# Kernel tuning notes

Hardware: AMD Instinct MI355X
Metric: run time of the kernel (lower is better)

Reference implementation:

```python
import jax, jax.numpy as jnp
import numpy as np

DIM = 2048
N_HEADS = 16
HEAD_DIM = DIM // N_HEADS  # 128
MAX_LEN = 2048
B, T = 2, 2048
RESTORE_SCALE = DIM ** 0.5  # sqkinit / sqkscale = 1 / (1/sqrt(dim))
SQK_SCALE = 1.0 / DIM ** 0.5


def _rope_tables(seq_len, head_dim, dtype=jnp.float32):
    d2 = head_dim // 2
    pos = jnp.arange(seq_len, dtype=dtype)                     # [T]
    theta = 1.0 / (10000.0 ** (jnp.arange(0, head_dim, 2, dtype=dtype) / head_dim))  # [d2]
    ang = pos[:, None] * theta[None, :]                        # [T, d2]
    return jnp.cos(ang), jnp.sin(ang)


def _apply_rope(x, cos, sin):
    # x: [B, H, T, D]; cos/sin: [T, D/2] broadcast over B,H
    d2 = x.shape[-1] // 2
    xr, xi = x[..., :d2], x[..., d2:]
    return jnp.concatenate([xr * cos - xi * sin, xr * sin + xi * cos], axis=-1)


def setup_inputs() -> dict:
    key = jax.random.key(0)
    ks = jax.random.split(key, 5)
    s = 0.02
    return {
        "x":  jax.random.normal(ks[0], (B, T, DIM), jnp.float32),
        "Wq": jax.random.normal(ks[1], (DIM, DIM), jnp.float32) * s,
        "Wk": jax.random.normal(ks[2], (DIM, DIM), jnp.float32) * s,
        "Wv": jax.random.normal(ks[3], (DIM, DIM), jnp.float32) * s,
        "Wo": jax.random.normal(ks[4], (DIM, DIM), jnp.float32) * s,
        "sqk": jnp.ones((N_HEADS, 1, HEAD_DIM), jnp.float32) * SQK_SCALE,
    }


def reference(x, Wq, Wk, Wv, Wo, sqk):
    Bc, Tc, C = x.shape
    # QKV projections (torch Linear: x @ W.T), split heads -> [B, H, T, D]
    def proj(W):
        return (x @ W.T).reshape(Bc, Tc, N_HEADS, HEAD_DIM).transpose(0, 2, 1, 3)
    q, k, v = proj(Wq), proj(Wk), proj(Wv)

    cos, sin = _rope_tables(Tc, HEAD_DIM, x.dtype)
    actual_sqk = sqk * RESTORE_SCALE  # [H, 1, D]
    q = _apply_rope(q, cos, sin) * actual_sqk
    k = _apply_rope(k, cos, sin) * actual_sqk

    # SDPA with scale = sqrt(head_dim) (as in the source, not 1/sqrt)
    scale = HEAD_DIM ** 0.5
    scores = jnp.einsum("bhtd,bhsd->bhts", q, k) * scale  # [B, H, T, T]
    causal = jnp.tril(jnp.ones((Tc, Tc), bool))
    scores = jnp.where(causal, scores, -jnp.inf)
    attn = jax.nn.softmax(scores, axis=-1)
    out = jnp.einsum("bhts,bhsd->bhtd", attn, v)           # [B, H, T, D]
    out = out.transpose(0, 2, 1, 3).reshape(Bc, Tc, C)

    y = out @ Wo.T
    # F.normalize(p=2, dim=-1, eps=1e-12)
    norm = jnp.linalg.norm(y, axis=-1, keepdims=True)
    return y / jnp.maximum(norm, 1e-12)
```

## Files before the change

### kernel.cpp

```cpp
#include <hip/hip_runtime.h>

#define DEVFN __device__ __forceinline__

typedef float    floatx4 __attribute__((ext_vector_type(4)));
typedef _Float16 half8   __attribute__((ext_vector_type(8)));
typedef _Float16 half4v  __attribute__((ext_vector_type(4)));

#define MFMA16H(a, b, c) __builtin_amdgcn_mfma_f32_16x16x32_f16((a), (b), (c), 0, 0, 0)

DEVFN void async16(void* lds, const void* g) {
  __builtin_amdgcn_global_load_lds(
      (const __attribute__((address_space(1))) unsigned int*)g,
      (__attribute__((address_space(3))) unsigned int*)lds, 16, 0, 0);
}
DEVFN half8 ld8h(const _Float16* p) { return *(const half8*)p; }

__global__ __launch_bounds__(256) void cvt_prep(
    const float4* __restrict__ x, const float4* __restrict__ wq,
    const float4* __restrict__ wk, const float4* __restrict__ wv,
    const float4* __restrict__ wo,
    half4v* __restrict__ xh, half4v* __restrict__ xl,
    half4v* __restrict__ qo, half4v* __restrict__ ko,
    half4v* __restrict__ vo, half4v* __restrict__ oo,
    float* __restrict__ cosT, float* __restrict__ sinT) {
  int i = blockIdx.x * 256 + threadIdx.x;
  {
    float4 v = x[i];
    half4v h = {(_Float16)v.x, (_Float16)v.y, (_Float16)v.z, (_Float16)v.w};
    half4v l = {(_Float16)(v.x - (float)h.x), (_Float16)(v.y - (float)h.y),
                (_Float16)(v.z - (float)h.z), (_Float16)(v.w - (float)h.w)};
    xh[i] = h;
    xl[i] = l;
  }
  if (i < 1048576) {
    float4 v = wq[i];
    qo[i] = (half4v){(_Float16)v.x, (_Float16)v.y, (_Float16)v.z, (_Float16)v.w};
    v = wk[i];
    ko[i] = (half4v){(_Float16)v.x, (_Float16)v.y, (_Float16)v.z, (_Float16)v.w};
    v = wv[i];
    vo[i] = (half4v){(_Float16)v.x, (_Float16)v.y, (_Float16)v.z, (_Float16)v.w};
    v = wo[i];
    oo[i] = (half4v){(_Float16)v.x, (_Float16)v.y, (_Float16)v.z, (_Float16)v.w};
  }
  if (i < 131072) {
    int t = i >> 6, d = i & 63;
    double theta = exp(-((double)(2 * d) / 128.0) * log(10000.0));
    double ang = (double)t * theta;
    cosT[i] = (float)cos(ang);
    sinT[i] = (float)sin(ang);
  }
}

__global__ __launch_bounds__(256, 2) void gemm_qkv_f16(
    const _Float16* __restrict__ xhp, const _Float16* __restrict__ xlp,
    const _Float16* __restrict__ wq, const _Float16* __restrict__ wk,
    const _Float16* __restrict__ wv,
    const float* __restrict__ cosT, const float* __restrict__ sinT,
    const float* __restrict__ sqk,
    _Float16* __restrict__ qhi, _Float16* __restrict__ qlo,
    _Float16* __restrict__ khi, _Float16* __restrict__ vo) {
  constexpr int Kd = 2048;
  const int n0 = blockIdx.x * 128, m0 = blockIdx.y * 128;
  const int tid = threadIdx.x, w = tid >> 6, lane = tid & 63;
  const int quad = lane >> 4, l16 = lane & 15;

  __shared__ __align__(16) _Float16 smem[5 * 4096];
  _Float16* Xh = smem;
  _Float16* Xl = smem + 4096;
  _Float16* Qs = smem + 8192;
  _Float16* Ks = smem + 12288;
  _Float16* Vs = smem + 16384;
  _Float16* stH = smem + w * 2176;
  _Float16* stL = smem + 8704 + w * 2176;

  floatx4 accQ[2][8], accK[2][8], accV[2][8];
#pragma unroll
  for (int i = 0; i < 2; i++)
#pragma unroll
    for (int j = 0; j < 8; j++) {
      accQ[i][j] = (floatx4){0.f, 0.f, 0.f, 0.f};
      accK[i][j] = (floatx4){0.f, 0.f, 0.f, 0.f};
      accV[i][j] = (floatx4){0.f, 0.f, 0.f, 0.f};
    }

  const int t0 = 2 * w, t1 = 2 * w + 1;
  const size_t xo0 = (size_t)(m0 + t0 * 16 + l16) * Kd + quad * 8;
  const size_t xo1 = (size_t)(m0 + t1 * 16 + l16) * Kd + quad * 8;
  const size_t wo0 = (size_t)(n0 + t0 * 16 + l16) * Kd + quad * 8;
  const size_t wo1 = (size_t)(n0 + t1 * 16 + l16) * Kd + quad * 8;

  for (int k0 = 0; k0 < Kd; k0 += 32) {
    __syncthreads();
    async16(&Xh[t0 * 512], xhp + xo0 + k0);
    async16(&Xh[t1 * 512], xhp + xo1 + k0);
    async16(&Xl[t0 * 512], xlp + xo0 + k0);
    async16(&Xl[t1 * 512], xlp + xo1 + k0);
    async16(&Qs[t0 * 512], wq + wo0 + k0);
    async16(&Qs[t1 * 512], wq + wo1 + k0);
    async16(&Ks[t0 * 512], wk + wo0 + k0);
    async16(&Ks[t1 * 512], wk + wo1 + k0);
    async16(&Vs[t0 * 512], wv + wo0 + k0);
    async16(&Vs[t1 * 512], wv + wo1 + k0);
    __syncthreads();
    half8 ah0 = ld8h(&Xh[t0 * 512 + lane * 8]);
    half8 ah1 = ld8h(&Xh[t1 * 512 + lane * 8]);
    half8 al0 = ld8h(&Xl[t0 * 512 + lane * 8]);
    half8 al1 = ld8h(&Xl[t1 * 512 + lane * 8]);
#pragma unroll
    for (int j = 0; j < 8; j++) {
      half8 b;
      b = ld8h(&Qs[j * 512 + lane * 8]);
      accQ[0][j] = MFMA16H(ah0, b, accQ[0][j]);
      accQ[1][j] = MFMA16H(ah1, b, accQ[1][j]);
      accQ[0][j] = MFMA16H(al0, b, accQ[0][j]);
      accQ[1][j] = MFMA16H(al1, b, accQ[1][j]);
      b = ld8h(&Ks[j * 512 + lane * 8]);
      accK[0][j] = MFMA16H(ah0, b, accK[0][j]);
      accK[1][j] = MFMA16H(ah1, b, accK[1][j]);
      accK[0][j] = MFMA16H(al0, b, accK[0][j]);
      accK[1][j] = MFMA16H(al1, b, accK[1][j]);
      b = ld8h(&Vs[j * 512 + lane * 8]);
      accV[0][j] = MFMA16H(ah0, b, accV[0][j]);
      accV[1][j] = MFMA16H(ah1, b, accV[1][j]);
    }
  }

  __syncthreads();

  const int h = n0 >> 7;
#pragma unroll
  for (int i = 0; i < 2; i++) {
    const int grow0 = m0 + (2 * w + i) * 16;
    const int bb = grow0 >> 11, tt0 = grow0 & 2047;
    const size_t gbase = (((size_t)(bb * 16 + h)) * 2048 + tt0) * 128;

#pragma unroll
    for (int j = 0; j < 4; j++) {
      int d = j * 16 + l16;
      float s1 = sqk[h * 128 + d] * 512.0f;
      float s2 = sqk[h * 128 + d + 64] * 512.0f;
#pragma unroll
      for (int r = 0; r < 4; r++) {
        int t = tt0 + quad * 4 + r;
        float c = cosT[t * 64 + d], s = sinT[t * 64 + d];
        float xr = accQ[i][j][r], xi = accQ[i][j + 4][r];
        float o1 = (xr * c - xi * s) * s1;
        float o2 = (xr * s + xi * c) * s2;
        _Float16 h1 = (_Float16)o1, h2 = (_Float16)o2;
        int rl = quad * 4 + r;
        stH[rl * 136 + d] = h1;
        stH[rl * 136 + d + 64] = h2;
        stL[rl * 136 + d] = (_Float16)(o1 - (float)h1);
        stL[rl * 136 + d + 64] = (_Float16)(o2 - (float)h2);
      }
    }
#pragma unroll
    for (int it = 0; it < 4; it++) {
      int pb = it * 1024 + lane * 16;
      int rr = pb >> 8, cs = (pb & 255) >> 1;
      *(half8*)(qhi + gbase + rr * 128 + cs) = ld8h(&stH[rr * 136 + cs]);
      *(half8*)(qlo + gbase + rr * 128 + cs) = ld8h(&stL[rr * 136 + cs]);
    }

#pragma unroll
    for (int j = 0; j < 4; j++) {
      int d = j * 16 + l16;
      float s1 = sqk[h * 128 + d] * 45.254834f;
      float s2 = sqk[h * 128 + d + 64] * 45.254834f;
#pragma unroll
      for (int r = 0; r < 4; r++) {
        int t = tt0 + quad * 4 + r;
        float c = cosT[t * 64 + d], s = sinT[t * 64 + d];
        float xr = accK[i][j][r], xi = accK[i][j + 4][r];
        int rl = quad * 4 + r;
        stH[rl * 136 + d] = (_Float16)((xr * c - xi * s) * s1);
        stH[rl * 136 + d + 64] = (_Float16)((xr * s + xi * c) * s2);
      }
    }
#pragma unroll
    for (int it = 0; it < 4; it++) {
      int pb = it * 1024 + lane * 16;
      int rr = pb >> 8, cs = (pb & 255) >> 1;
      *(half8*)(khi + gbase + rr * 128 + cs) = ld8h(&stH[rr * 136 + cs]);
    }

#pragma unroll
    for (int j = 0; j < 8; j++)
#pragma unroll
      for (int r = 0; r < 4; r++)
        stH[(quad * 4 + r) * 136 + j * 16 + l16] = (_Float16)accV[i][j][r];
#pragma unroll
    for (int it = 0; it < 4; it++) {
      int pb = it * 1024 + lane * 16;
      int rr = pb >> 8, cs = (pb & 255) >> 1;
      *(half8*)(vo + gbase + rr * 128 + cs) = ld8h(&stH[rr * 136 + cs]);
    }
  }
}

__global__ __launch_bounds__(256) void transpose_v(
    const unsigned short* __restrict__ v, unsigned short* __restrict__ vt) {
  __shared__ unsigned short tile[32][33];
  int t0 = blockIdx.x * 32, d0 = blockIdx.y * 32, bh = blockIdx.z;
  int tx = threadIdx.x & 31, ty = threadIdx.x >> 5;
  for (int r = ty; r < 32; r += 8)
    tile[r][tx] = v[((size_t)bh * 2048 + t0 + r) * 128 + d0 + tx];
  __syncthreads();
  for (int r = ty; r < 32; r += 8)
    vt[((size_t)bh * 128 + d0 + r) * 2048 + t0 + tx] = tile[tx][r];
}

__global__ __launch_bounds__(256, 2) void flash_attn(
    const _Float16* __restrict__ qhp, const _Float16* __restrict__ qlp,
    const _Float16* __restrict__ khp,
    const _Float16* __restrict__ vtp, _Float16* __restrict__ aout) {
  constexpr int T = 2048, HD = 128;
  const int bh = blockIdx.x, qt = blockIdx.y;
  const int q0 = qt * 128;
  const int tid = threadIdx.x, w = tid >> 6, lane = tid & 63;
  const int quad = lane >> 4, l16 = lane & 15;

  __shared__ __align__(16) _Float16 Kh[8192];
  __shared__ __align__(16) _Float16 Vt[8192];
  __shared__ __align__(16) _Float16 Pb[4][16 * 72];

  const size_t qkbase = (size_t)bh * T * HD;

  half8 qh[2][4], ql[2][4];
#pragma unroll
  for (int i = 0; i < 2; i++)
#pragma unroll
    for (int s = 0; s < 4; s++) {
      size_t off = qkbase + (size_t)(q0 + w * 32 + i * 16 + l16) * HD + s * 32 + quad * 8;
      qh[i][s] = *(const half8*)(qhp + off);
      ql[i][s] = *(const half8*)(qlp + off);
    }

  floatx4 o[2][8];
#pragma unroll
  for (int i = 0; i < 2; i++)
#pragma unroll
    for (int dt = 0; dt < 8; dt++) o[i][dt] = (floatx4){0.f, 0.f, 0.f, 0.f};
  float mrow[2][4], lrow[2][4];
#pragma unroll
  for (int i = 0; i < 2; i++)
#pragma unroll
    for (int r = 0; r < 4; r++) { mrow[i][r] = -3e38f; lrow[i][r] = 0.f; }

  const int ntiles = q0 / 64 + 2;
  for (int kt = 0; kt < ntiles; ++kt) {
    const int s0 = kt * 64;
    __syncthreads();
    for (int c = w; c < 16; c += 4) {
      int tt = c >> 2, ss = c & 3;
      size_t go = qkbase + (size_t)(s0 + tt * 16 + l16) * HD + ss * 32 + quad * 8;
      async16(&Kh[c * 512], khp + go);
      int dt = c >> 1, vs = c & 1;
      size_t vo = (size_t)bh * HD * T + (size_t)(dt * 16 + l16) * T + s0 + vs * 32 + quad * 8;
      async16(&Vt[c * 512], vtp + vo);
    }
    __syncthreads();

    floatx4 S[2][4];
#pragma unroll
    for (int i = 0; i < 2; i++)
#pragma unroll
      for (int j = 0; j < 4; j++) S[i][j] = (floatx4){0.f, 0.f, 0.f, 0.f};

#pragma unroll
    for (int s = 0; s < 4; s++) {
#pragma unroll
      for (int j = 0; j < 4; j++) {
        half8 kh = ld8h(&Kh[(j * 4 + s) * 512 + lane * 8]);
        S[0][j] = MFMA16H(qh[0][s], kh, S[0][j]);
        S[1][j] = MFMA16H(qh[1][s], kh, S[1][j]);
        S[0][j] = MFMA16H(ql[0][s], kh, S[0][j]);
        S[1][j] = MFMA16H(ql[1][s], kh, S[1][j]);
      }
    }

    if (s0 + 63 > q0) {
#pragma unroll
      for (int i = 0; i < 2; i++) {
        int rb = q0 + w * 32 + i * 16 + quad * 4;
#pragma unroll
        for (int j = 0; j < 4; j++) {
          int cg = s0 + j * 16 + l16;
#pragma unroll
          for (int r = 0; r < 4; r++)
            if (cg > rb + r) S[i][j][r] = -3e38f;
        }
      }
    }

    half8 pf[2][2];
#pragma unroll
    for (int i = 0; i < 2; i++) {
#pragma unroll
      for (int r = 0; r < 4; r++) {
        float mx = fmaxf(fmaxf(S[i][0][r], S[i][1][r]), fmaxf(S[i][2][r], S[i][3][r]));
#pragma unroll
        for (int d = 1; d < 16; d <<= 1) mx = fmaxf(mx, __shfl_xor(mx, d, 64));
        float mnew = fmaxf(mrow[i][r], mx);
        float al = __expf(mrow[i][r] - mnew);
        mrow[i][r] = mnew;
        float sum = 0.f;
#pragma unroll
        for (int j = 0; j < 4; j++) {
          float p = __expf(S[i][j][r] - mnew);
          S[i][j][r] = p;
          sum += p;
        }
#pragma unroll
        for (int d = 1; d < 16; d <<= 1) sum += __shfl_xor(sum, d, 64);
        lrow[i][r] = lrow[i][r] * al + sum;
#pragma unroll
        for (int dt = 0; dt < 8; dt++) o[i][dt][r] *= al;
      }
#pragma unroll
      for (int r = 0; r < 4; r++)
#pragma unroll
        for (int j = 0; j < 4; j++)
          Pb[w][(quad * 4 + r) * 72 + j * 16 + l16] = (_Float16)S[i][j][r];
      pf[i][0] = ld8h(&Pb[w][l16 * 72 + quad * 8]);
      pf[i][1] = ld8h(&Pb[w][l16 * 72 + 32 + quad * 8]);
    }

#pragma unroll
    for (int dt = 0; dt < 8; dt++) {
#pragma unroll
      for (int s = 0; s < 2; s++) {
        half8 vf = ld8h(&Vt[(dt * 2 + s) * 512 + lane * 8]);
        o[0][dt] = MFMA16H(pf[0][s], vf, o[0][dt]);
        o[1][dt] = MFMA16H(pf[1][s], vf, o[1][dt]);
      }
    }
  }

  const int b = bh >> 4, h = bh & 15;
#pragma unroll
  for (int i = 0; i < 2; i++) {
#pragma unroll
    for (int r = 0; r < 4; r++) {
      int trow = q0 + w * 32 + i * 16 + quad * 4 + r;
      float linv = 1.0f / lrow[i][r];
      size_t base = ((size_t)(b * T + trow)) * 2048 + h * 128;
#pragma unroll
      for (int dt = 0; dt < 8; dt++)
        aout[base + dt * 16 + l16] = (_Float16)(o[i][dt][r] * linv);
    }
  }
}

__global__ __launch_bounds__(256, 2) void gemm_o_f16(
    const _Float16* __restrict__ A, const _Float16* __restrict__ B,
    float* __restrict__ outF) {
  constexpr int Kd = 2048;
  constexpr int Nd = 2048;
  const int n0 = blockIdx.x * 128, m0 = blockIdx.y * 128;
  const int tid = threadIdx.x, w = tid >> 6, lane = tid & 63;
  const int quad = lane >> 4, l16 = lane & 15;

  __shared__ __align__(16) _Float16 As[8192];
  __shared__ __align__(16) _Float16 Bs[8192];

  floatx4 acc[2][8];
#pragma unroll
  for (int i = 0; i < 2; i++)
#pragma unroll
    for (int j = 0; j < 8; j++) acc[i][j] = (floatx4){0.f, 0.f, 0.f, 0.f};

  const int t0 = 2 * w, t1 = 2 * w + 1;
  const size_t ao0 = (size_t)(m0 + t0 * 16 + l16) * Kd + quad * 8;
  const size_t ao1 = (size_t)(m0 + t1 * 16 + l16) * Kd + quad * 8;
  const size_t bo0 = (size_t)(n0 + t0 * 16 + l16) * Kd + quad * 8;
  const size_t bo1 = (size_t)(n0 + t1 * 16 + l16) * Kd + quad * 8;

  for (int k0 = 0; k0 < Kd; k0 += 64) {
    __syncthreads();
    async16(&As[t0 * 512], A + ao0 + k0);
    async16(&As[t1 * 512], A + ao1 + k0);
    async16(&As[4096 + t0 * 512], A + ao0 + k0 + 32);
    async16(&As[4096 + t1 * 512], A + ao1 + k0 + 32);
    async16(&Bs[t0 * 512], B + bo0 + k0);
    async16(&Bs[t1 * 512], B + bo1 + k0);
    async16(&Bs[4096 + t0 * 512], B + bo0 + k0 + 32);
    async16(&Bs[4096 + t1 * 512], B + bo1 + k0 + 32);
    __syncthreads();
    half8 a00 = ld8h(&As[t0 * 512 + lane * 8]);
    half8 a10 = ld8h(&As[t1 * 512 + lane * 8]);
    half8 a01 = ld8h(&As[4096 + t0 * 512 + lane * 8]);
    half8 a11 = ld8h(&As[4096 + t1 * 512 + lane * 8]);
#pragma unroll
    for (int j = 0; j < 8; j++) {
      half8 b0 = ld8h(&Bs[j * 512 + lane * 8]);
      acc[0][j] = MFMA16H(a00, b0, acc[0][j]);
      acc[1][j] = MFMA16H(a10, b0, acc[1][j]);
      half8 b1 = ld8h(&Bs[4096 + j * 512 + lane * 8]);
      acc[0][j] = MFMA16H(a01, b1, acc[0][j]);
      acc[1][j] = MFMA16H(a11, b1, acc[1][j]);
    }
  }

#pragma unroll
  for (int i = 0; i < 2; i++) {
    int rbase = m0 + (2 * w + i) * 16 + quad * 4;
#pragma unroll
    for (int j = 0; j < 8; j++) {
      int col = n0 + j * 16 + l16;
#pragma unroll
      for (int r = 0; r < 4; r++)
        outF[(size_t)(rbase + r) * Nd + col] = acc[i][j][r];
    }
  }
}

__global__ __launch_bounds__(256) void rownorm(const float* __restrict__ y,
                                               float* __restrict__ out) {
  int row = blockIdx.x;
  const float4* yr = (const float4*)(y + (size_t)row * 2048);
  float4* od = (float4*)(out + (size_t)row * 2048);
  int t = threadIdx.x;
  float4 v0 = yr[t], v1 = yr[t + 256];
  float ss = v0.x * v0.x + v0.y * v0.y + v0.z * v0.z + v0.w * v0.w +
             v1.x * v1.x + v1.y * v1.y + v1.z * v1.z + v1.w * v1.w;
#pragma unroll
  for (int d = 1; d < 64; d <<= 1) ss += __shfl_xor(ss, d, 64);
  __shared__ float red[4];
  if ((t & 63) == 0) red[t >> 6] = ss;
  __syncthreads();
  float tot = red[0] + red[1] + red[2] + red[3];
  float inv = 1.0f / fmaxf(sqrtf(tot), 1e-12f);
  v0.x *= inv; v0.y *= inv; v0.z *= inv; v0.w *= inv;
  v1.x *= inv; v1.y *= inv; v1.z *= inv; v1.w *= inv;
  od[t] = v0;
  od[t + 256] = v1;
}

extern "C" void kernel_launch(void* const* d_in, const int* in_sizes, int n_in,
                              void* d_out, int out_size, void* d_ws, size_t ws_size,
                              hipStream_t stream) {
  (void)in_sizes; (void)n_in; (void)out_size; (void)ws_size;
  const float* x   = (const float*)d_in[0];
  const float* Wq  = (const float*)d_in[1];
  const float* Wk  = (const float*)d_in[2];
  const float* Wv  = (const float*)d_in[3];
  const float* Wo  = (const float*)d_in[4];
  const float* sqk = (const float*)d_in[5];
  char* ws = (char*)d_ws;

  constexpr size_t SZX = 8388608ull * 2;
  constexpr size_t SZW = 4194304ull * 2;

  size_t o_xh = 0;
  size_t o_xl = o_xh + SZX;
  size_t o_wq = o_xl + SZX;
  size_t o_wk = o_wq + SZW;
  size_t o_wv = o_wk + SZW;
  size_t o_wo = o_wv + SZW;
  size_t o_qh = o_wo + SZW;
  size_t o_ql = o_qh + SZX;
  size_t o_kh = o_ql + SZX;
  size_t o_v  = o_kh + SZX;
  size_t o_vt = o_v + SZX;
  size_t o_cos = o_vt + SZX;
  size_t o_sin = o_cos + 2048 * 64 * 4;
  size_t o_aout = o_wq;
  size_t o_y    = o_qh;

  _Float16* xh = (_Float16*)(ws + o_xh);
  _Float16* xl = (_Float16*)(ws + o_xl);
  _Float16* wq = (_Float16*)(ws + o_wq);
  _Float16* wk = (_Float16*)(ws + o_wk);
  _Float16* wv = (_Float16*)(ws + o_wv);
  _Float16* wo = (_Float16*)(ws + o_wo);
  _Float16* qh = (_Float16*)(ws + o_qh);
  _Float16* ql = (_Float16*)(ws + o_ql);
  _Float16* kh = (_Float16*)(ws + o_kh);
  _Float16* v  = (_Float16*)(ws + o_v);
  _Float16* vt = (_Float16*)(ws + o_vt);
  float* cosT = (float*)(ws + o_cos);
  float* sinT = (float*)(ws + o_sin);
  _Float16* aout = (_Float16*)(ws + o_aout);
  float* y = (float*)(ws + o_y);

  cvt_prep<<<8192, 256, 0, stream>>>((const float4*)x, (const float4*)Wq,
                                     (const float4*)Wk, (const float4*)Wv,
                                     (const float4*)Wo, (half4v*)xh, (half4v*)xl,
                                     (half4v*)wq, (half4v*)wk, (half4v*)wv,
                                     (half4v*)wo, cosT, sinT);

  gemm_qkv_f16<<<dim3(16, 32), 256, 0, stream>>>(xh, xl, wq, wk, wv, cosT,
                                                 sinT, sqk, qh, ql, kh, v);
  transpose_v<<<dim3(64, 4, 32), 256, 0, stream>>>((const unsigned short*)v,
                                                   (unsigned short*)vt);

  flash_attn<<<dim3(32, 16), 256, 0, stream>>>(qh, ql, kh, vt, aout);

  gemm_o_f16<<<dim3(16, 32), 256, 0, stream>>>(aout, wo, y);
  rownorm<<<4096, 256, 0, stream>>>(y, (float*)d_out);
}
```

Before: 531.5 us.

## Triple-buffer QKV GEMM with async prefetch, 8 waves and phased MFMA scheduling

Rewrites the fused QKV projection GEMM to use 512 threads (8 waves, one 16-row tile each) and a three-stage LDS ring buffer. Global-to-LDS async loads for tile k+2 are issued in interleaved phases while MFMAs on the current tile run, with explicit vmcnt waits, barriers and setprio to overlap memory with compute. This targets the load-then-sync stall of the old single-buffered loop. The cost is 120 KB of LDS per block, which limits blocks per CU, plus hand-tuned waitcnt logic that could be fragile.

```diff
diff --git a/kernel.cpp b/kernel.cpp
--- a/kernel.cpp
+++ b/kernel.cpp
@@ -51,7 +51,7 @@
   }
 }
 
-__global__ __launch_bounds__(256, 2) void gemm_qkv_f16(
+__global__ __launch_bounds__(512, 2) void gemm_qkv_f16(
     const _Float16* __restrict__ xhp, const _Float16* __restrict__ xlp,
     const _Float16* __restrict__ wq, const _Float16* __restrict__ wk,
     const _Float16* __restrict__ wv,
@@ -59,143 +59,181 @@
     const float* __restrict__ sqk,
     _Float16* __restrict__ qhi, _Float16* __restrict__ qlo,
     _Float16* __restrict__ khi, _Float16* __restrict__ vo) {
-  constexpr int Kd = 2048;
+  constexpr int Kd = 2048, NT = 64;
   const int n0 = blockIdx.x * 128, m0 = blockIdx.y * 128;
   const int tid = threadIdx.x, w = tid >> 6, lane = tid & 63;
   const int quad = lane >> 4, l16 = lane & 15;
 
-  __shared__ __align__(16) _Float16 smem[5 * 4096];
-  _Float16* Xh = smem;
-  _Float16* Xl = smem + 4096;
-  _Float16* Qs = smem + 8192;
-  _Float16* Ks = smem + 12288;
-  _Float16* Vs = smem + 16384;
+  __shared__ __align__(16) _Float16 smem[61440];
+#define BUF(b) (smem + (b) * 20480)
+
+  floatx4 accQ[8], accK[8], accV[8];
+#pragma unroll
+  for (int j = 0; j < 8; j++) {
+    accQ[j] = (floatx4){0.f, 0.f, 0.f, 0.f};
+    accK[j] = (floatx4){0.f, 0.f, 0.f, 0.f};
+    accV[j] = (floatx4){0.f, 0.f, 0.f, 0.f};
+  }
+
+  const size_t xoff = (size_t)(m0 + w * 16 + l16) * Kd + quad * 8;
+  const size_t woff = (size_t)(n0 + w * 16 + l16) * Kd + quad * 8;
+
+  async16(BUF(0) + w * 512,         xhp + xoff);
+  async16(BUF(0) + 4096 + w * 512,  xlp + xoff);
+  async16(BUF(0) + 8192 + w * 512,  wq + woff);
+  async16(BUF(0) + 12288 + w * 512, wk + woff);
+  async16(BUF(0) + 16384 + w * 512, wv + woff);
+  async16(BUF(1) + w * 512,         xhp + xoff + 32);
+  async16(BUF(1) + 4096 + w * 512,  xlp + xoff + 32);
+  async16(BUF(1) + 8192 + w * 512,  wq + woff + 32);
+  async16(BUF(1) + 12288 + w * 512, wk + woff + 32);
+  async16(BUF(1) + 16384 + w * 512, wv + woff + 32);
+  asm volatile("s_waitcnt vmcnt(5)" ::: "memory");
+  __builtin_amdgcn_s_barrier();
+
+#define QKV_PHASE(J0, STAGE)                                        \
+  {                                                                 \
+    half8 bq0 = ld8h(qs_ + (J0) * 512 + lane * 8);                  \
+    half8 bq1 = ld8h(qs_ + ((J0) + 1) * 512 + lane * 8);            \
+    half8 bk0 = ld8h(ks_ + (J0) * 512 + lane * 8);                  \
+    half8 bk1 = ld8h(ks_ + ((J0) + 1) * 512 + lane * 8);            \
+    half8 bv0 = ld8h(vs_ + (J0) * 512 + lane * 8);                  \
+    half8 bv1 = ld8h(vs_ + ((J0) + 1) * 512 + lane * 8);            \
+    STAGE;                                                          \
+    __builtin_amdgcn_s_barrier();                                   \
+    asm volatile("s_waitcnt lgkmcnt(0)");                           \
+    __builtin_amdgcn_sched_barrier(0);                              \
+    __builtin_amdgcn_s_setprio(1);                                  \
+    accQ[(J0)] = MFMA16H(ah, bq0, accQ[(J0)]);                      \
+    accQ[(J0) + 1] = MFMA16H(ah, bq1, accQ[(J0) + 1]);              \
+    accK[(J0)] = MFMA16H(ah, bk0, accK[(J0)]);                      \
+    accK[(J0) + 1] = MFMA16H(ah, bk1, accK[(J0) + 1]);              \
+    accV[(J0)] = MFMA16H(ah, bv0, accV[(J0)]);                      \
+    accV[(J0) + 1] = MFMA16H(ah, bv1, accV[(J0) + 1]);              \
+    accQ[(J0)] = MFMA16H(al, bq0, accQ[(J0)]);                      \
+    accQ[(J0) + 1] = MFMA16H(al, bq1, accQ[(J0) + 1]);              \
+    accK[(J0)] = MFMA16H(al, bk0, accK[(J0)]);                      \
+    accK[(J0) + 1] = MFMA16H(al, bk1, accK[(J0) + 1]);              \
+    __builtin_amdgcn_s_setprio(0);                                  \
+  }
+
+  int cur = 0;
+#pragma unroll 1
+  for (int t = 0; t < NT; ++t) {
+    const _Float16* xh_ = BUF(cur);
+    const _Float16* xl_ = BUF(cur) + 4096;
+    const _Float16* qs_ = BUF(cur) + 8192;
+    const _Float16* ks_ = BUF(cur) + 12288;
+    const _Float16* vs_ = BUF(cur) + 16384;
+    int nb = cur - 1;
+    if (nb < 0) nb = 2;
+    _Float16* nxt = BUF(nb);
+    const bool pre = t < NT - 2;
+    const int kpre = (t + 2) * 32;
+    half8 ah, al;
+
+    QKV_PHASE(0,
+      ah = ld8h(xh_ + w * 512 + lane * 8);
+      al = ld8h(xl_ + w * 512 + lane * 8);
+      if (pre) {
+        async16(nxt + w * 512, xhp + xoff + kpre);
+        async16(nxt + 4096 + w * 512, xlp + xoff + kpre);
+      }
+    );
+    __builtin_amdgcn_s_barrier();
+    QKV_PHASE(2,
+      if (pre) { async16(nxt + 8192 + w * 512, wq + woff + kpre); }
+    );
+    __builtin_amdgcn_s_barrier();
+    QKV_PHASE(4,
+      if (pre) { async16(nxt + 12288 + w * 512, wk + woff + kpre); }
+    );
+    __builtin_amdgcn_s_barrier();
+    QKV_PHASE(6,
+      if (pre) { async16(nxt + 16384 + w * 512, wv + woff + kpre); }
+    );
+    if (pre) {
+      asm volatile("s_waitcnt vmcnt(5)" ::: "memory");
+    } else {
+      asm volatile("s_waitcnt vmcnt(0)" ::: "memory");
+    }
+    __builtin_amdgcn_s_barrier();
+    cur++;
+    if (cur == 3) cur = 0;
+  }
+#undef QKV_PHASE
+
+  __syncthreads();
   _Float16* stH = smem + w * 2176;
-  _Float16* stL = smem + 8704 + w * 2176;
-
-  floatx4 accQ[2][8], accK[2][8], accV[2][8];
-#pragma unroll
-  for (int i = 0; i < 2; i++)
-#pragma unroll
-    for (int j = 0; j < 8; j++) {
-      accQ[i][j] = (floatx4){0.f, 0.f, 0.f, 0.f};
-      accK[i][j] = (floatx4){0.f, 0.f, 0.f, 0.f};
-      accV[i][j] = (floatx4){0.f, 0.f, 0.f, 0.f};
-    }
-
-  const int t0 = 2 * w, t1 = 2 * w + 1;
-  const size_t xo0 = (size_t)(m0 + t0 * 16 + l16) * Kd + quad * 8;
-  const size_t xo1 = (size_t)(m0 + t1 * 16 + l16) * Kd + quad * 8;
-  const size_t wo0 = (size_t)(n0 + t0 * 16 + l16) * Kd + quad * 8;
-  const size_t wo1 = (size_t)(n0 + t1 * 16 + l16) * Kd + quad * 8;
-
-  for (int k0 = 0; k0 < Kd; k0 += 32) {
-    __syncthreads();
-    async16(&Xh[t0 * 512], xhp + xo0 + k0);
-    async16(&Xh[t1 * 512], xhp + xo1 + k0);
-    async16(&Xl[t0 * 512], xlp + xo0 + k0);
-    async16(&Xl[t1 * 512], xlp + xo1 + k0);
-    async16(&Qs[t0 * 512], wq + wo0 + k0);
-    async16(&Qs[t1 * 512], wq + wo1 + k0);
-    async16(&Ks[t0 * 512], wk + wo0 + k0);
-    async16(&Ks[t1 * 512], wk + wo1 + k0);
-    async16(&Vs[t0 * 512], wv + wo0 + k0);
-    async16(&Vs[t1 * 512], wv + wo1 + k0);
-    __syncthreads();
-    half8 ah0 = ld8h(&Xh[t0 * 512 + lane * 8]);
-    half8 ah1 = ld8h(&Xh[t1 * 512 + lane * 8]);
-    half8 al0 = ld8h(&Xl[t0 * 512 + lane * 8]);
-    half8 al1 = ld8h(&Xl[t1 * 512 + lane * 8]);
-#pragma unroll
-    for (int j = 0; j < 8; j++) {
-      half8 b;
-      b = ld8h(&Qs[j * 512 + lane * 8]);
-      accQ[0][j] = MFMA16H(ah0, b, accQ[0][j]);
-      accQ[1][j] = MFMA16H(ah1, b, accQ[1][j]);
-      accQ[0][j] = MFMA16H(al0, b, accQ[0][j]);
-      accQ[1][j] = MFMA16H(al1, b, accQ[1][j]);
-      b = ld8h(&Ks[j * 512 + lane * 8]);
-      accK[0][j] = MFMA16H(ah0, b, accK[0][j]);
-      accK[1][j] = MFMA16H(ah1, b, accK[1][j]);
-      accK[0][j] = MFMA16H(al0, b, accK[0][j]);
-      accK[1][j] = MFMA16H(al1, b, accK[1][j]);
-      b = ld8h(&Vs[j * 512 + lane * 8]);
-      accV[0][j] = MFMA16H(ah0, b, accV[0][j]);
-      accV[1][j] = MFMA16H(ah1, b, accV[1][j]);
-    }
-  }
-
-  __syncthreads();
+  _Float16* stL = smem + 17408 + w * 2176;
 
   const int h = n0 >> 7;
-#pragma unroll
-  for (int i = 0; i < 2; i++) {
-    const int grow0 = m0 + (2 * w + i) * 16;
-    const int bb = grow0 >> 11, tt0 = grow0 & 2047;
-    const size_t gbase = (((size_t)(bb * 16 + h)) * 2048 + tt0) * 128;
-
-#pragma unroll
-    for (int j = 0; j < 4; j++) {
-      int d = j * 16 + l16;
-      float s1 = sqk[h * 128 + d] * 512.0f;
-      float s2 = sqk[h * 128 + d + 64] * 512.0f;
-#pragma unroll
-      for (int r = 0; r < 4; r++) {
-        int t = tt0 + quad * 4 + r;
-        float c = cosT[t * 64 + d], s = sinT[t * 64 + d];
-        float xr = accQ[i][j][r], xi = accQ[i][j + 4][r];
-        float o1 = (xr * c - xi * s) * s1;
-        float o2 = (xr * s + xi * c) * s2;
-        _Float16 h1 = (_Float16)o1, h2 = (_Float16)o2;
-        int rl = quad * 4 + r;
-        stH[rl * 136 + d] = h1;
-        stH[rl * 136 + d + 64] = h2;
-        stL[rl * 136 + d] = (_Float16)(o1 - (float)h1);
-        stL[rl * 136 + d + 64] = (_Float16)(o2 - (float)h2);
-      }
-    }
-#pragma unroll
-    for (int it = 0; it < 4; it++) {
-      int pb = it * 1024 + lane * 16;
-      int rr = pb >> 8, cs = (pb & 255) >> 1;
-      *(half8*)(qhi + gbase + rr * 128 + cs) = ld8h(&stH[rr * 136 + cs]);
-      *(half8*)(qlo + gbase + rr * 128 + cs) = ld8h(&stL[rr * 136 + cs]);
-    }
-
-#pragma unroll
-    for (int j = 0; j < 4; j++) {
-      int d = j * 16 + l16;
-      float s1 = sqk[h * 128 + d] * 45.254834f;
-      float s2 = sqk[h * 128 + d + 64] * 45.254834f;
-#pragma unroll
-      for (int r = 0; r < 4; r++) {
-        int t = tt0 + quad * 4 + r;
-        float c = cosT[t * 64 + d], s = sinT[t * 64 + d];
-        float xr = accK[i][j][r], xi = accK[i][j + 4][r];
-        int rl = quad * 4 + r;
-        stH[rl * 136 + d] = (_Float16)((xr * c - xi * s) * s1);
-        stH[rl * 136 + d + 64] = (_Float16)((xr * s + xi * c) * s2);
-      }
-    }
-#pragma unroll
-    for (int it = 0; it < 4; it++) {
-      int pb = it * 1024 + lane * 16;
-      int rr = pb >> 8, cs = (pb & 255) >> 1;
-      *(half8*)(khi + gbase + rr * 128 + cs) = ld8h(&stH[rr * 136 + cs]);
-    }
-
-#pragma unroll
-    for (int j = 0; j < 8; j++)
-#pragma unroll
-      for (int r = 0; r < 4; r++)
-        stH[(quad * 4 + r) * 136 + j * 16 + l16] = (_Float16)accV[i][j][r];
-#pragma unroll
-    for (int it = 0; it < 4; it++) {
-      int pb = it * 1024 + lane * 16;
-      int rr = pb >> 8, cs = (pb & 255) >> 1;
-      *(half8*)(vo + gbase + rr * 128 + cs) = ld8h(&stH[rr * 136 + cs]);
-    }
-  }
+  const int grow0 = m0 + w * 16;
+  const int bb = grow0 >> 11, tt0 = grow0 & 2047;
+  const size_t gbase = (((size_t)(bb * 16 + h)) * 2048 + tt0) * 128;
+
+#pragma unroll
+  for (int j = 0; j < 4; j++) {
+    int d = j * 16 + l16;
+    float s1 = sqk[h * 128 + d] * 512.0f;
+    float s2 = sqk[h * 128 + d + 64] * 512.0f;
+#pragma unroll
+    for (int r = 0; r < 4; r++) {
+      int tq = tt0 + quad * 4 + r;
+      float c = cosT[tq * 64 + d], s = sinT[tq * 64 + d];
+      float xr = accQ[j][r], xi = accQ[j + 4][r];
+      float o1 = (xr * c - xi * s) * s1;
+      float o2 = (xr * s + xi * c) * s2;
+      _Float16 h1 = (_Float16)o1, h2 = (_Float16)o2;
+      int rl = quad * 4 + r;
+      stH[rl * 136 + d] = h1;
+      stH[rl * 136 + d + 64] = h2;
+      stL[rl * 136 + d] = (_Float16)(o1 - (float)h1);
+      stL[rl * 136 + d + 64] = (_Float16)(o2 - (float)h2);
+    }
+  }
+#pragma unroll
+  for (int it = 0; it < 4; it++) {
+    int pbyte = it * 1024 + lane * 16;
+    int rr = pbyte >> 8, cs = (pbyte & 255) >> 1;
+    *(half8*)(qhi + gbase + rr * 128 + cs) = ld8h(&stH[rr * 136 + cs]);
+    *(half8*)(qlo + gbase + rr * 128 + cs) = ld8h(&stL[rr * 136 + cs]);
+  }
+
+#pragma unroll
+  for (int j = 0; j < 4; j++) {
+    int d = j * 16 + l16;
+    float s1 = sqk[h * 128 + d] * 45.254834f;
+    float s2 = sqk[h * 128 + d + 64] * 45.254834f;
+#pragma unroll
+    for (int r = 0; r < 4; r++) {
+      int tq = tt0 + quad * 4 + r;
+      float c = cosT[tq * 64 + d], s = sinT[tq * 64 + d];
+      float xr = accK[j][r], xi = accK[j + 4][r];
+      int rl = quad * 4 + r;
+      stH[rl * 136 + d] = (_Float16)((xr * c - xi * s) * s1);
+      stH[rl * 136 + d + 64] = (_Float16)((xr * s + xi * c) * s2);
+    }
+  }
+#pragma unroll
+  for (int it = 0; it < 4; it++) {
+    int pbyte = it * 1024 + lane * 16;
+    int rr = pbyte >> 8, cs = (pbyte & 255) >> 1;
+    *(half8*)(khi + gbase + rr * 128 + cs) = ld8h(&stH[rr * 136 + cs]);
+  }
+
+#pragma unroll
+  for (int j = 0; j < 8; j++)
+#pragma unroll
+    for (int r = 0; r < 4; r++)
+      stH[(quad * 4 + r) * 136 + j * 16 + l16] = (_Float16)accV[j][r];
+#pragma unroll
+  for (int it = 0; it < 4; it++) {
+    int pbyte = it * 1024 + lane * 16;
+    int rr = pbyte >> 8, cs = (pbyte & 255) >> 1;
+    *(half8*)(vo + gbase + rr * 128 + cs) = ld8h(&stH[rr * 136 + cs]);
+  }
+#undef BUF
 }
 
 __global__ __launch_bounds__(256) void transpose_v(
@@ -490,7 +528,7 @@
                                      (half4v*)wq, (half4v*)wk, (half4v*)wv,
                                      (half4v*)wo, cosT, sinT);
 
-  gemm_qkv_f16<<<dim3(16, 32), 256, 0, stream>>>(xh, xl, wq, wk, wv, cosT,
+  gemm_qkv_f16<<<dim3(16, 32), 512, 0, stream>>>(xh, xl, wq, wk, wv, cosT,
                                                  sinT, sqk, qh, ql, kh, v);
   transpose_v<<<dim3(64, 4, 32), 256, 0, stream>>>((const unsigned short*)v,
                                                    (unsigned short*)vt);
```

Result: no change. 535.8 us (+0.8%).
